# Optimization experiments

Measured on AMD Instinct MI355X. Metric: run time of the kernel, lower is better.

Reference implementation:

```python
import jax, jax.numpy as jnp
import numpy as np

B, K, D = 4096, 16, 256
NUM_CODES = 512
BETA = 0.25  # commitment (activation_entropy=None path)
LN_EPS = 1e-5

def setup_inputs() -> dict:
    key = jax.random.key(0)
    ks = jax.random.split(key, 6)
    hidden = jax.random.normal(ks[0], (B, K, D), dtype=jnp.float32)
    active_mask = jax.random.randint(ks[1], (B, K), 0, 2).astype(bool)
    bound = 1.0 / NUM_CODES
    codebook = jax.random.uniform(ks[2], (NUM_CODES, D), minval=-bound, maxval=bound, dtype=jnp.float32)
    lim = 1.0 / np.sqrt(D)
    W_in = jax.random.uniform(ks[3], (D, D), minval=-lim, maxval=lim, dtype=jnp.float32)
    W_out = jax.random.uniform(ks[4], (D, D), minval=-lim, maxval=lim, dtype=jnp.float32)
    ln_gamma = jnp.ones((D,), jnp.float32)
    ln_beta = jnp.zeros((D,), jnp.float32)
    return {"hidden": hidden, "active_mask": active_mask, "codebook": codebook,
            "W_in": W_in, "W_out": W_out, "ln_gamma": ln_gamma, "ln_beta": ln_beta}

def reference(hidden, active_mask, codebook, W_in, W_out, ln_gamma, ln_beta):
    sg = jax.lax.stop_gradient
    z = jnp.einsum('bkd,ed->bke', hidden, W_in)              # proj_in (no bias)
    z_flat = z.reshape(-1, D)                                 # [B*K, D]
    # ||z - c||^2 = |z|^2 - 2 z.c + |c|^2
    dist = (jnp.sum(z_flat * z_flat, -1, keepdims=True)
            - 2.0 * z_flat @ codebook.T
            + jnp.sum(codebook * codebook, -1))               # [B*K, C]
    idx = jnp.argmin(dist, axis=-1)                           # [B*K]
    z_q = codebook[idx].reshape(z.shape)                      # gather
    vq_loss = jnp.mean((sg(z_q) - z) ** 2) + BETA * jnp.mean((z_q - sg(z)) ** 2)
    z_st = z + sg(z_q - z)                                    # straight-through
    out = jnp.einsum('bkd,ed->bke', z_st, W_out)              # proj_out
    h = hidden + active_mask[..., None].astype(jnp.float32) * out
    mu = jnp.mean(h, -1, keepdims=True)
    var = jnp.mean((h - mu) ** 2, -1, keepdims=True)
    h_comm = (h - mu) * jax.lax.rsqrt(var + LN_EPS) * ln_gamma + ln_beta
    return h_comm, vq_loss
```

## Files before the change

### kernel.cpp

```cpp
#include <hip/hip_runtime.h>

#define LN_EPS 1e-5f

typedef short bf16x8 __attribute__((ext_vector_type(8)));
typedef float f32x4  __attribute__((ext_vector_type(4)));

__device__ __forceinline__ unsigned short f2bf(float f) {
  unsigned u = __float_as_uint(f);
  u += 0x7fffu + ((u >> 16) & 1u);
  return (unsigned short)(u >> 16);
}
__device__ __forceinline__ float bf2f(unsigned short s) {
  return __uint_as_float(((unsigned)s) << 16);
}

__device__ __forceinline__ bf16x8 pack8(float4 a, float4 b) {
  bf16x8 v;
  v[0] = (short)f2bf(a.x); v[1] = (short)f2bf(a.y);
  v[2] = (short)f2bf(a.z); v[3] = (short)f2bf(a.w);
  v[4] = (short)f2bf(b.x); v[5] = (short)f2bf(b.y);
  v[6] = (short)f2bf(b.z); v[7] = (short)f2bf(b.w);
  return v;
}

__global__ __launch_bounds__(256) void prep_kernel(
    const float* __restrict__ codebook, const float* __restrict__ W_in,
    const float* __restrict__ W_out,
    float* __restrict__ loss_acc, unsigned* __restrict__ ticket,
    float* __restrict__ c2, float* __restrict__ code_out,
    unsigned short* __restrict__ BT) {
  const int b = blockIdx.x, t = threadIdx.x;
  if (b < 32) {
    if (b == 0 && t == 0) { *loss_acc = 0.f; *ticket = 0u; }
    int e = b * 8 + (t >> 5);
    int c32 = t & 31, ks = c32 >> 2, kq = c32 & 3;
    const float* src = W_in + e * 256 + c32 * 8;
    float4 x0 = *(const float4*)src, x1 = *(const float4*)(src + 4);
    *(bf16x8*)(BT + ks * 8192 + (e >> 6) * 2048 + ((e >> 4) & 3) * 512 +
               kq * 128 + (e & 15) * 8) = pack8(x0, x1);
  } else if (b < 96) {
    int code = (b - 32) * 8 + (t >> 5);
    int c32 = t & 31, ks = c32 >> 2, kq = c32 & 3;
    const float* src = codebook + code * 256 + c32 * 8;
    float4 x0 = *(const float4*)src, x1 = *(const float4*)(src + 4);
    int cl = code & 255;
    int chunk = 8 + (code >> 8) * 8 + ks;
    *(bf16x8*)(BT + chunk * 8192 + (cl >> 6) * 2048 + ((cl >> 4) & 3) * 512 +
               kq * 128 + (cl & 15) * 8) = pack8(x0, x1);
    float s = x0.x * x0.x + x0.y * x0.y + x0.z * x0.z + x0.w * x0.w +
              x1.x * x1.x + x1.y * x1.y + x1.z * x1.z + x1.w * x1.w;
    s += __shfl_xor(s, 1);  s += __shfl_xor(s, 2);
    s += __shfl_xor(s, 4);  s += __shfl_xor(s, 8);
    s += __shfl_xor(s, 16);
    if ((t & 31) == 0) c2[code] = s;
  } else {
    __shared__ float Cs[32][260];
    __shared__ float Ws[16][260];
    int bi = b - 96, ci = bi & 15, ei = bi >> 4;
    {
      int row = t >> 4, col = (t & 15) * 16;
      const float4* s = (const float4*)(W_out + (size_t)(ei * 16 + row) * 256 + col);
      float4* d = (float4*)&Ws[row][col];
      d[0] = s[0]; d[1] = s[1]; d[2] = s[2]; d[3] = s[3];
    }
    {
      int row = t >> 3, col = (t & 7) * 32;
      const float4* s = (const float4*)(codebook + (size_t)(ci * 32 + row) * 256 + col);
      float4* d = (float4*)&Cs[row][col];
      #pragma unroll
      for (int k = 0; k < 8; k++) d[k] = s[k];
    }
    __syncthreads();
    int c = t & 31, e0 = t >> 5;
    float a0 = 0.f, a1 = 0.f;
    #pragma unroll 4
    for (int d = 0; d < 256; d += 4) {
      float4 cv = *(const float4*)&Cs[c][d];
      float4 w0 = *(const float4*)&Ws[e0][d];
      float4 w1 = *(const float4*)&Ws[e0 + 8][d];
      a0 += cv.x * w0.x + cv.y * w0.y + cv.z * w0.z + cv.w * w0.w;
      a1 += cv.x * w1.x + cv.y * w1.y + cv.z * w1.z + cv.w * w1.w;
    }
    code_out[(size_t)(ci * 32 + c) * 256 + ei * 16 + e0]     = a0;
    code_out[(size_t)(ci * 32 + c) * 256 + ei * 16 + e0 + 8] = a1;
  }
}

__global__ __launch_bounds__(512, 4) void main_kernel(
    const float* __restrict__ hidden, const int* __restrict__ mask,
    const float* __restrict__ gamma, const float* __restrict__ beta,
    const float* __restrict__ c2g, const float* __restrict__ code_out,
    const unsigned short* __restrict__ BT,
    float* __restrict__ loss_acc, unsigned* __restrict__ ticket,
    float* __restrict__ out) {

  __shared__ unsigned short HZ[64 * 264];
  __shared__ float    z2[64];
  __shared__ unsigned sminp[512];
  __shared__ int      ridx[64];

  const int t    = threadIdx.x;
  const int lane = t & 63;
  const int w    = t >> 6;
  const int l15  = lane & 15;
  const int quad = lane >> 4;
  const int row0 = blockIdx.x * 64;

  float ccp[2][2];
  #pragma unroll
  for (int p = 0; p < 2; p++)
    #pragma unroll
    for (int j = 0; j < 2; j++)
      ccp[p][j] = c2g[p * 256 + w * 32 + j * 16 + l15];

  {
    #pragma unroll
    for (int i = 0; i < 4; i++) {
      int flat = (t * 8) + i * 4096;
      int r = flat >> 8, c = flat & 255;
      const float* src = hidden + (size_t)row0 * 256 + flat;
      float4 x0 = *(const float4*)src, x1 = *(const float4*)(src + 4);
      *(bf16x8*)(HZ + r * 264 + c) = pack8(x0, x1);
    }
  }
  __syncthreads();

  const f32x4 zf = {0.f, 0.f, 0.f, 0.f};
  f32x4 acc[4][2];
  #pragma unroll
  for (int i = 0; i < 4; i++)
    #pragma unroll
    for (int j = 0; j < 2; j++) acc[i][j] = zf;

  const unsigned short* BTw = BT + w * 1024 + lane * 8;

  #pragma unroll 2
  for (int ks = 0; ks < 8; ks++) {
    const unsigned short* bp = BTw + ks * 8192;
    bf16x8 b0 = *(const bf16x8*)(bp);
    bf16x8 b1 = *(const bf16x8*)(bp + 512);
    bf16x8 a[4];
    #pragma unroll
    for (int i = 0; i < 4; i++)
      a[i] = *(const bf16x8*)(HZ + (i * 16 + l15) * 264 + ks * 32 + quad * 8);
    #pragma unroll
    for (int i = 0; i < 4; i++) {
      acc[i][0] = __builtin_amdgcn_mfma_f32_16x16x32_bf16(a[i], b0, acc[i][0], 0, 0, 0);
      acc[i][1] = __builtin_amdgcn_mfma_f32_16x16x32_bf16(a[i], b1, acc[i][1], 0, 0, 0);
    }
  }

  __syncthreads();
  #pragma unroll
  for (int i = 0; i < 4; i++)
    #pragma unroll
    for (int j = 0; j < 2; j++)
      #pragma unroll
      for (int r = 0; r < 4; r++)
        HZ[(i * 16 + quad * 4 + r) * 264 + (w * 32 + j * 16 + l15)] =
            f2bf(acc[i][j][r]);
  __syncthreads();

  {
    int zr = t >> 3, part = t & 7;
    float s = 0.f;
    const unsigned short* zp = HZ + zr * 264 + part * 32;
    #pragma unroll
    for (int c = 0; c < 32; c += 8) {
      bf16x8 v = *(const bf16x8*)(zp + c);
      #pragma unroll
      for (int e = 0; e < 8; e++) { float f = bf2f((unsigned short)v[e]); s += f * f; }
    }
    s += __shfl_xor(s, 1);
    s += __shfl_xor(s, 2);
    s += __shfl_xor(s, 4);
    if (part == 0) z2[zr] = s;
  }

  unsigned runp[16];
  #pragma unroll
  for (int r = 0; r < 16; r++) runp[r] = 0xFFFFFFFFu;

  #pragma unroll
  for (int pass = 0; pass < 2; pass++) {
    #pragma unroll
    for (int i = 0; i < 4; i++)
      #pragma unroll
      for (int j = 0; j < 2; j++) acc[i][j] = zf;

    #pragma unroll 2
    for (int ks = 0; ks < 8; ks++) {
      const unsigned short* bp = BTw + (8 + pass * 8 + ks) * 8192;
      bf16x8 b0 = *(const bf16x8*)(bp);
      bf16x8 b1 = *(const bf16x8*)(bp + 512);
      bf16x8 a[4];
      #pragma unroll
      for (int i = 0; i < 4; i++)
        a[i] = *(const bf16x8*)(HZ + (i * 16 + l15) * 264 + ks * 32 + quad * 8);
      #pragma unroll
      for (int i = 0; i < 4; i++) {
        acc[i][0] = __builtin_amdgcn_mfma_f32_16x16x32_bf16(a[i], b0, acc[i][0], 0, 0, 0);
        acc[i][1] = __builtin_amdgcn_mfma_f32_16x16x32_bf16(a[i], b1, acc[i][1], 0, 0, 0);
      }
    }
    #pragma unroll
    for (int i = 0; i < 4; i++)
      #pragma unroll
      for (int j = 0; j < 2; j++) {
        int code = pass * 256 + w * 32 + j * 16 + l15;
        float cc = ccp[pass][j];
        #pragma unroll
        for (int r = 0; r < 4; r++) {
          float m = cc - 2.f * acc[i][j][r];
          unsigned bits = __float_as_uint(m);
          unsigned u = bits ^ (0x80000000u | (unsigned)((int)bits >> 31));
          unsigned p = (u & 0xFFFFFE00u) | (unsigned)code;
          int ri = i * 4 + r;
          runp[ri] = min(runp[ri], p);
        }
      }
  }

  #pragma unroll
  for (int ri = 0; ri < 16; ri++) {
    unsigned v = runp[ri];
    v = min(v, (unsigned)__shfl_xor((int)v, 1));
    v = min(v, (unsigned)__shfl_xor((int)v, 2));
    v = min(v, (unsigned)__shfl_xor((int)v, 4));
    v = min(v, (unsigned)__shfl_xor((int)v, 8));
    if (l15 == 0) {
      int i = ri >> 2, r = ri & 3;
      sminp[w * 64 + (i * 16 + quad * 4 + r)] = v;
    }
  }
  __syncthreads();

  if (t < 64) {
    int row = t;
    unsigned bv = sminp[row];
    #pragma unroll
    for (int ww = 1; ww < 8; ww++) bv = min(bv, sminp[ww * 64 + row]);
    ridx[row] = (int)(bv & 511u);
    unsigned u = bv & 0xFFFFFE00u;
    unsigned bits = (u & 0x80000000u) ? (u ^ 0x80000000u) : ~u;
    float dist = z2[row] + __uint_as_float(bits);
    #pragma unroll
    for (int m = 1; m < 64; m <<= 1) dist += __shfl_xor(dist, m);
    if (t == 0) {
      atomicAdd(loss_acc, dist);
      __threadfence();
      unsigned done = atomicAdd(ticket, 1u);
      if (done == gridDim.x - 1) {
        float total = atomicAdd(loss_acc, 0.f);
        out[16777216] = 1.25f * total * (1.f / 16777216.f);
      }
    }
  }
  __syncthreads();

  {
    float4 g4 = *(const float4*)(gamma + lane * 4);
    float4 b4 = *(const float4*)(beta + lane * 4);
    for (int rr = 0; rr < 8; rr++) {
      int row = w * 8 + rr;
      int gr  = row0 + row;
      float4 h = *(const float4*)(hidden + (size_t)gr * 256 + lane * 4);
      int code = ridx[row];
      float4 o = *(const float4*)(code_out + (size_t)code * 256 + lane * 4);
      float mf = mask[gr] ? 1.f : 0.f;
      h.x += mf * o.x; h.y += mf * o.y; h.z += mf * o.z; h.w += mf * o.w;
      float s  = h.x + h.y + h.z + h.w;
      float sq = h.x * h.x + h.y * h.y + h.z * h.z + h.w * h.w;
      #pragma unroll
      for (int m = 1; m < 64; m <<= 1) { s += __shfl_xor(s, m); sq += __shfl_xor(sq, m); }
      float mean = s * (1.f / 256.f);
      float var  = sq * (1.f / 256.f) - mean * mean;
      float rstd = rsqrtf(var + LN_EPS);
      float4 res;
      res.x = (h.x - mean) * rstd * g4.x + b4.x;
      res.y = (h.y - mean) * rstd * g4.y + b4.y;
      res.z = (h.z - mean) * rstd * g4.z + b4.z;
      res.w = (h.w - mean) * rstd * g4.w + b4.w;
      *(float4*)(out + (size_t)gr * 256 + lane * 4) = res;
    }
  }
}

extern "C" void kernel_launch(void* const* d_in, const int* in_sizes, int n_in,
                              void* d_out, int out_size, void* d_ws, size_t ws_size,
                              hipStream_t stream) {
  (void)in_sizes; (void)n_in; (void)out_size; (void)ws_size;
  const float* hidden   = (const float*)d_in[0];
  const int*   mask     = (const int*)d_in[1];
  const float* codebook = (const float*)d_in[2];
  const float* W_in     = (const float*)d_in[3];
  const float* W_out    = (const float*)d_in[4];
  const float* gamma    = (const float*)d_in[5];
  const float* beta     = (const float*)d_in[6];
  float* out = (float*)d_out;

  float* wsf      = (float*)d_ws;
  float* loss_acc = wsf;
  unsigned* ticket = (unsigned*)(wsf + 1);
  float* c2       = wsf + 64;
  float* code_out = wsf + 64 + 512;
  unsigned short* BT = (unsigned short*)(wsf + 64 + 512 + 512 * 256);

  prep_kernel<<<352, 256, 0, stream>>>(codebook, W_in, W_out, loss_acc, ticket,
                                       c2, code_out, BT);
  main_kernel<<<1024, 512, 0, stream>>>(hidden, mask, gamma, beta, c2, code_out,
                                        BT, loss_acc, ticket, out);
}
```

Baseline: 184.8 us.

## Fold W_in into codebook and compute z-norm via W_in Gram matrix

The prep kernel now precomputes codebook·W_in (the codebook projected back into hidden space) and the Gram matrix W_inᵀW_in, both stored as bf16 MFMA operand tiles. The main kernel computes code distances directly from the hidden rows, skipping the explicit z = hidden·W_in projection and its LDS write-back. The |z|^2 term for the loss becomes hᵀ(W_inᵀW_in)h, evaluated with one extra MFMA pass against the Gram tiles. This swaps one projection GEMM plus a round trip through shared memory for a Gram GEMM of the same size, and adds two small fp32 GEMMs to the prep kernel. Rounding now happens on different intermediates, so argmin ties and the loss value may shift slightly.

```diff
diff --git a/kernel.cpp b/kernel.cpp
--- a/kernel.cpp
+++ b/kernel.cpp
@@ -30,43 +30,36 @@
     float* __restrict__ c2, float* __restrict__ code_out,
     unsigned short* __restrict__ BT) {
   const int b = blockIdx.x, t = threadIdx.x;
-  if (b < 32) {
+  __shared__ float As[32][260];
+  __shared__ float Bs[16][260];
+  __shared__ float Res[32][17];
+
+  if (b < 64) {
     if (b == 0 && t == 0) { *loss_acc = 0.f; *ticket = 0u; }
-    int e = b * 8 + (t >> 5);
-    int c32 = t & 31, ks = c32 >> 2, kq = c32 & 3;
-    const float* src = W_in + e * 256 + c32 * 8;
+    int code = b * 8 + (t >> 5);
+    const float* src = codebook + (size_t)code * 256 + (t & 31) * 8;
     float4 x0 = *(const float4*)src, x1 = *(const float4*)(src + 4);
-    *(bf16x8*)(BT + ks * 8192 + (e >> 6) * 2048 + ((e >> 4) & 3) * 512 +
-               kq * 128 + (e & 15) * 8) = pack8(x0, x1);
-  } else if (b < 96) {
-    int code = (b - 32) * 8 + (t >> 5);
-    int c32 = t & 31, ks = c32 >> 2, kq = c32 & 3;
-    const float* src = codebook + code * 256 + c32 * 8;
-    float4 x0 = *(const float4*)src, x1 = *(const float4*)(src + 4);
-    int cl = code & 255;
-    int chunk = 8 + (code >> 8) * 8 + ks;
-    *(bf16x8*)(BT + chunk * 8192 + (cl >> 6) * 2048 + ((cl >> 4) & 3) * 512 +
-               kq * 128 + (cl & 15) * 8) = pack8(x0, x1);
     float s = x0.x * x0.x + x0.y * x0.y + x0.z * x0.z + x0.w * x0.w +
               x1.x * x1.x + x1.y * x1.y + x1.z * x1.z + x1.w * x1.w;
     s += __shfl_xor(s, 1);  s += __shfl_xor(s, 2);
     s += __shfl_xor(s, 4);  s += __shfl_xor(s, 8);
     s += __shfl_xor(s, 16);
     if ((t & 31) == 0) c2[code] = s;
-  } else {
-    __shared__ float Cs[32][260];
-    __shared__ float Ws[16][260];
-    int bi = b - 96, ci = bi & 15, ei = bi >> 4;
+    return;
+  }
+
+  if (b < 320) {
+    int bi = b - 64, ci = bi & 15, ei = bi >> 4;
     {
       int row = t >> 4, col = (t & 15) * 16;
       const float4* s = (const float4*)(W_out + (size_t)(ei * 16 + row) * 256 + col);
-      float4* d = (float4*)&Ws[row][col];
+      float4* d = (float4*)&Bs[row][col];
       d[0] = s[0]; d[1] = s[1]; d[2] = s[2]; d[3] = s[3];
     }
     {
       int row = t >> 3, col = (t & 7) * 32;
       const float4* s = (const float4*)(codebook + (size_t)(ci * 32 + row) * 256 + col);
-      float4* d = (float4*)&Cs[row][col];
+      float4* d = (float4*)&As[row][col];
       #pragma unroll
       for (int k = 0; k < 8; k++) d[k] = s[k];
     }
@@ -75,14 +68,113 @@
     float a0 = 0.f, a1 = 0.f;
     #pragma unroll 4
     for (int d = 0; d < 256; d += 4) {
-      float4 cv = *(const float4*)&Cs[c][d];
-      float4 w0 = *(const float4*)&Ws[e0][d];
-      float4 w1 = *(const float4*)&Ws[e0 + 8][d];
+      float4 cv = *(const float4*)&As[c][d];
+      float4 w0 = *(const float4*)&Bs[e0][d];
+      float4 w1 = *(const float4*)&Bs[e0 + 8][d];
       a0 += cv.x * w0.x + cv.y * w0.y + cv.z * w0.z + cv.w * w0.w;
       a1 += cv.x * w1.x + cv.y * w1.y + cv.z * w1.z + cv.w * w1.w;
     }
     code_out[(size_t)(ci * 32 + c) * 256 + ei * 16 + e0]     = a0;
     code_out[(size_t)(ci * 32 + c) * 256 + ei * 16 + e0 + 8] = a1;
+    return;
+  }
+
+  if (b < 576) {
+    int bi = b - 320, ci = bi & 15, di = bi >> 4;
+    int c0 = ci * 32, d0 = di * 16;
+    {
+      int e = t;
+      const float* src = W_in + (size_t)e * 256 + d0;
+      #pragma unroll
+      for (int k = 0; k < 4; k++) {
+        float4 v = *(const float4*)(src + k * 4);
+        Bs[k * 4 + 0][e] = v.x; Bs[k * 4 + 1][e] = v.y;
+        Bs[k * 4 + 2][e] = v.z; Bs[k * 4 + 3][e] = v.w;
+      }
+    }
+    {
+      int row = t >> 3, col = (t & 7) * 32;
+      const float4* s = (const float4*)(codebook + (size_t)(c0 + row) * 256 + col);
+      float4* d = (float4*)&As[row][col];
+      #pragma unroll
+      for (int k = 0; k < 8; k++) d[k] = s[k];
+    }
+    __syncthreads();
+    int c = t & 31, dl = t >> 5;
+    float a0 = 0.f, a1 = 0.f;
+    #pragma unroll 4
+    for (int d = 0; d < 256; d += 4) {
+      float4 cv = *(const float4*)&As[c][d];
+      float4 w0 = *(const float4*)&Bs[dl][d];
+      float4 w1 = *(const float4*)&Bs[dl + 8][d];
+      a0 += cv.x * w0.x + cv.y * w0.y + cv.z * w0.z + cv.w * w0.w;
+      a1 += cv.x * w1.x + cv.y * w1.y + cv.z * w1.z + cv.w * w1.w;
+    }
+    Res[c][dl] = a0; Res[c][dl + 8] = a1;
+    __syncthreads();
+    if (t < 64) {
+      int c2i = t & 31, kqo = t >> 5;
+      int code = c0 + c2i, dg = d0 + kqo * 8;
+      int cl = code & 255;
+      int chunk = (code >> 8) * 8 + (dg >> 5);
+      int kq = (dg >> 3) & 3;
+      float4 x0, x1;
+      x0.x = Res[c2i][kqo * 8 + 0]; x0.y = Res[c2i][kqo * 8 + 1];
+      x0.z = Res[c2i][kqo * 8 + 2]; x0.w = Res[c2i][kqo * 8 + 3];
+      x1.x = Res[c2i][kqo * 8 + 4]; x1.y = Res[c2i][kqo * 8 + 5];
+      x1.z = Res[c2i][kqo * 8 + 6]; x1.w = Res[c2i][kqo * 8 + 7];
+      *(bf16x8*)(BT + chunk * 8192 + (cl >> 4) * 512 + kq * 128 + (cl & 15) * 8) =
+          pack8(x0, x1);
+    }
+    return;
+  }
+
+  {
+    int bi = b - 576;
+    int ks = bi & 7, bt = bi >> 3;
+    int a0c = ks * 32, b0c = bt * 16;
+    {
+      int e = t;
+      const float* srca = W_in + (size_t)e * 256 + a0c;
+      #pragma unroll
+      for (int k = 0; k < 8; k++) {
+        float4 v = *(const float4*)(srca + k * 4);
+        As[k * 4 + 0][e] = v.x; As[k * 4 + 1][e] = v.y;
+        As[k * 4 + 2][e] = v.z; As[k * 4 + 3][e] = v.w;
+      }
+      const float* srcb = W_in + (size_t)e * 256 + b0c;
+      #pragma unroll
+      for (int k = 0; k < 4; k++) {
+        float4 v = *(const float4*)(srcb + k * 4);
+        Bs[k * 4 + 0][e] = v.x; Bs[k * 4 + 1][e] = v.y;
+        Bs[k * 4 + 2][e] = v.z; Bs[k * 4 + 3][e] = v.w;
+      }
+    }
+    __syncthreads();
+    int al = t & 31, bl = t >> 5;
+    float s0 = 0.f, s1 = 0.f;
+    #pragma unroll 4
+    for (int d = 0; d < 256; d += 4) {
+      float4 av = *(const float4*)&As[al][d];
+      float4 w0 = *(const float4*)&Bs[bl][d];
+      float4 w1 = *(const float4*)&Bs[bl + 8][d];
+      s0 += av.x * w0.x + av.y * w0.y + av.z * w0.z + av.w * w0.w;
+      s1 += av.x * w1.x + av.y * w1.y + av.z * w1.z + av.w * w1.w;
+    }
+    Res[al][bl] = s0; Res[al][bl + 8] = s1;
+    __syncthreads();
+    if (t < 64) {
+      int bcol = t & 15, kqo = t >> 4;
+      int cl = b0c + bcol;
+      int chunk = 16 + ks;
+      float4 x0, x1;
+      x0.x = Res[kqo * 8 + 0][bcol]; x0.y = Res[kqo * 8 + 1][bcol];
+      x0.z = Res[kqo * 8 + 2][bcol]; x0.w = Res[kqo * 8 + 3][bcol];
+      x1.x = Res[kqo * 8 + 4][bcol]; x1.y = Res[kqo * 8 + 5][bcol];
+      x1.z = Res[kqo * 8 + 6][bcol]; x1.w = Res[kqo * 8 + 7][bcol];
+      *(bf16x8*)(BT + chunk * 8192 + (cl >> 4) * 512 + kqo * 128 + (cl & 15) * 8) =
+          pack8(x0, x1);
+    }
   }
 }
 
@@ -94,9 +186,9 @@
     float* __restrict__ loss_acc, unsigned* __restrict__ ticket,
     float* __restrict__ out) {
 
-  __shared__ unsigned short HZ[64 * 264];
-  __shared__ float    z2[64];
+  __shared__ unsigned short H[64 * 264];
   __shared__ unsigned sminp[512];
+  __shared__ float    lossw[8];
   __shared__ int      ridx[64];
 
   const int t    = threadIdx.x;
@@ -113,73 +205,24 @@
     for (int j = 0; j < 2; j++)
       ccp[p][j] = c2g[p * 256 + w * 32 + j * 16 + l15];
 
-  {
-    #pragma unroll
-    for (int i = 0; i < 4; i++) {
-      int flat = (t * 8) + i * 4096;
-      int r = flat >> 8, c = flat & 255;
-      const float* src = hidden + (size_t)row0 * 256 + flat;
-      float4 x0 = *(const float4*)src, x1 = *(const float4*)(src + 4);
-      *(bf16x8*)(HZ + r * 264 + c) = pack8(x0, x1);
-    }
+  #pragma unroll
+  for (int i = 0; i < 4; i++) {
+    int flat = (t * 8) + i * 4096;
+    int r = flat >> 8, c = flat & 255;
+    const float* src = hidden + (size_t)row0 * 256 + flat;
+    float4 x0 = *(const float4*)src, x1 = *(const float4*)(src + 4);
+    *(bf16x8*)(H + r * 264 + c) = pack8(x0, x1);
   }
   __syncthreads();
 
+  const unsigned short* BTw = BT + w * 1024 + lane * 8;
   const f32x4 zf = {0.f, 0.f, 0.f, 0.f};
+
+  unsigned runp[16];
+  #pragma unroll
+  for (int r = 0; r < 16; r++) runp[r] = 0xFFFFFFFFu;
+
   f32x4 acc[4][2];
-  #pragma unroll
-  for (int i = 0; i < 4; i++)
-    #pragma unroll
-    for (int j = 0; j < 2; j++) acc[i][j] = zf;
-
-  const unsigned short* BTw = BT + w * 1024 + lane * 8;
-
-  #pragma unroll 2
-  for (int ks = 0; ks < 8; ks++) {
-    const unsigned short* bp = BTw + ks * 8192;
-    bf16x8 b0 = *(const bf16x8*)(bp);
-    bf16x8 b1 = *(const bf16x8*)(bp + 512);
-    bf16x8 a[4];
-    #pragma unroll
-    for (int i = 0; i < 4; i++)
-      a[i] = *(const bf16x8*)(HZ + (i * 16 + l15) * 264 + ks * 32 + quad * 8);
-    #pragma unroll
-    for (int i = 0; i < 4; i++) {
-      acc[i][0] = __builtin_amdgcn_mfma_f32_16x16x32_bf16(a[i], b0, acc[i][0], 0, 0, 0);
-      acc[i][1] = __builtin_amdgcn_mfma_f32_16x16x32_bf16(a[i], b1, acc[i][1], 0, 0, 0);
-    }
-  }
-
-  __syncthreads();
-  #pragma unroll
-  for (int i = 0; i < 4; i++)
-    #pragma unroll
-    for (int j = 0; j < 2; j++)
-      #pragma unroll
-      for (int r = 0; r < 4; r++)
-        HZ[(i * 16 + quad * 4 + r) * 264 + (w * 32 + j * 16 + l15)] =
-            f2bf(acc[i][j][r]);
-  __syncthreads();
-
-  {
-    int zr = t >> 3, part = t & 7;
-    float s = 0.f;
-    const unsigned short* zp = HZ + zr * 264 + part * 32;
-    #pragma unroll
-    for (int c = 0; c < 32; c += 8) {
-      bf16x8 v = *(const bf16x8*)(zp + c);
-      #pragma unroll
-      for (int e = 0; e < 8; e++) { float f = bf2f((unsigned short)v[e]); s += f * f; }
-    }
-    s += __shfl_xor(s, 1);
-    s += __shfl_xor(s, 2);
-    s += __shfl_xor(s, 4);
-    if (part == 0) z2[zr] = s;
-  }
-
-  unsigned runp[16];
-  #pragma unroll
-  for (int r = 0; r < 16; r++) runp[r] = 0xFFFFFFFFu;
 
   #pragma unroll
   for (int pass = 0; pass < 2; pass++) {
@@ -190,13 +233,13 @@
 
     #pragma unroll 2
     for (int ks = 0; ks < 8; ks++) {
-      const unsigned short* bp = BTw + (8 + pass * 8 + ks) * 8192;
+      const unsigned short* bp = BTw + (pass * 8 + ks) * 8192;
       bf16x8 b0 = *(const bf16x8*)(bp);
       bf16x8 b1 = *(const bf16x8*)(bp + 512);
       bf16x8 a[4];
       #pragma unroll
       for (int i = 0; i < 4; i++)
-        a[i] = *(const bf16x8*)(HZ + (i * 16 + l15) * 264 + ks * 32 + quad * 8);
+        a[i] = *(const bf16x8*)(H + (i * 16 + l15) * 264 + ks * 32 + quad * 8);
       #pragma unroll
       for (int i = 0; i < 4; i++) {
         acc[i][0] = __builtin_amdgcn_mfma_f32_16x16x32_bf16(a[i], b0, acc[i][0], 0, 0, 0);
@@ -233,21 +276,61 @@
       sminp[w * 64 + (i * 16 + quad * 4 + r)] = v;
     }
   }
+
+  #pragma unroll
+  for (int i = 0; i < 4; i++)
+    #pragma unroll
+    for (int j = 0; j < 2; j++) acc[i][j] = zf;
+
+  #pragma unroll 2
+  for (int ks = 0; ks < 8; ks++) {
+    const unsigned short* gp = BTw + (16 + ks) * 8192;
+    bf16x8 g0 = *(const bf16x8*)(gp);
+    bf16x8 g1 = *(const bf16x8*)(gp + 512);
+    bf16x8 a[4];
+    #pragma unroll
+    for (int i = 0; i < 4; i++)
+      a[i] = *(const bf16x8*)(H + (i * 16 + l15) * 264 + ks * 32 + quad * 8);
+    #pragma unroll
+    for (int i = 0; i < 4; i++) {
+      acc[i][0] = __builtin_amdgcn_mfma_f32_16x16x32_bf16(g0, a[i], acc[i][0], 0, 0, 0);
+      acc[i][1] = __builtin_amdgcn_mfma_f32_16x16x32_bf16(g1, a[i], acc[i][1], 0, 0, 0);
+    }
+  }
+  {
+    float lsum = 0.f;
+    #pragma unroll
+    for (int i = 0; i < 4; i++)
+      #pragma unroll
+      for (int j = 0; j < 2; j++) {
+        const unsigned short* hp =
+            H + (i * 16 + l15) * 264 + w * 32 + j * 16 + quad * 4;
+        uint2 hv = *(const uint2*)hp;
+        lsum += acc[i][j][0] * bf2f((unsigned short)(hv.x & 0xFFFFu));
+        lsum += acc[i][j][1] * bf2f((unsigned short)(hv.x >> 16));
+        lsum += acc[i][j][2] * bf2f((unsigned short)(hv.y & 0xFFFFu));
+        lsum += acc[i][j][3] * bf2f((unsigned short)(hv.y >> 16));
+      }
+    #pragma unroll
+    for (int m = 1; m < 64; m <<= 1) lsum += __shfl_xor(lsum, m);
+    if (lane == 0) lossw[w] = lsum;
+  }
   __syncthreads();
 
   if (t < 64) {
-    int row = t;
-    unsigned bv = sminp[row];
-    #pragma unroll
-    for (int ww = 1; ww < 8; ww++) bv = min(bv, sminp[ww * 64 + row]);
-    ridx[row] = (int)(bv & 511u);
+    unsigned bv = sminp[t];
+    #pragma unroll
+    for (int ww = 1; ww < 8; ww++) bv = min(bv, sminp[ww * 64 + t]);
+    ridx[t] = (int)(bv & 511u);
     unsigned u = bv & 0xFFFFFE00u;
     unsigned bits = (u & 0x80000000u) ? (u ^ 0x80000000u) : ~u;
-    float dist = z2[row] + __uint_as_float(bits);
+    float dist = __uint_as_float(bits);
     #pragma unroll
     for (int m = 1; m < 64; m <<= 1) dist += __shfl_xor(dist, m);
     if (t == 0) {
-      atomicAdd(loss_acc, dist);
+      float lw = lossw[0] + lossw[1] + lossw[2] + lossw[3] +
+                 lossw[4] + lossw[5] + lossw[6] + lossw[7];
+      atomicAdd(loss_acc, dist + lw);
       __threadfence();
       unsigned done = atomicAdd(ticket, 1u);
       if (done == gridDim.x - 1) {
@@ -306,7 +389,7 @@
   float* code_out = wsf + 64 + 512;
   unsigned short* BT = (unsigned short*)(wsf + 64 + 512 + 512 * 256);
 
-  prep_kernel<<<352, 256, 0, stream>>>(codebook, W_in, W_out, loss_acc, ticket,
+  prep_kernel<<<704, 256, 0, stream>>>(codebook, W_in, W_out, loss_acc, ticket,
                                        c2, code_out, BT);
   main_kernel<<<1024, 512, 0, stream>>>(hidden, mask, gamma, beta, c2, code_out,
                                         BT, loss_acc, ticket, out);
```

New measurement: 197.2 us. 6.7% more time.
